# Kernel optimization log

Hardware: AMD Instinct MI355X
Metric: run time of the kernel (lower is better)

## Reference

```python
import jax, jax.numpy as jnp
import numpy as np

K = 16       # patchsize
STRIDE = 4
C1 = 1e-6
C2 = 1e-6


def _unfold(x):
    # Mirrors nn.Unfold(kernel_size=16, stride=4) followed by
    # .view(a,b,k,k,-1).transpose(2,4): output (a,b,pt_num,k,k) where the
    # trailing (k,k) matrix is the TRANSPOSED patch (kw,kh), exactly as in torch.
    a, b, H, W = x.shape
    nh = (H - K) // STRIDE + 1
    nw = (W - K) // STRIDE + 1
    r = (jnp.arange(nh) * STRIDE)[:, None] + jnp.arange(K)[None, :]  # (nh,K)
    c = (jnp.arange(nw) * STRIDE)[:, None] + jnp.arange(K)[None, :]  # (nw,K)
    p = x[:, :, r[:, None, :, None], c[None, :, None, :]]  # (a,b,nh,nw,K,K) = (kh,kw)
    p = p.reshape(a, b, nh * nw, K, K)
    return jnp.swapaxes(p, -1, -2)  # transposed patch, matching transpose(2,4)


def _layer(ref_f, dist_f):
    # ref_f, dist_f: (a,b,H,W) feature maps of one VGG layer
    pr = _unfold(ref_f)   # (a,b,pt,K,K)
    pd = _unfold(dist_f)
    u_r, s_r, _ = jnp.linalg.svd(pr, full_matrices=False)  # u:(a,b,pt,K,K) s:(a,b,pt,K)
    u_d, s_d, _ = jnp.linalg.svd(pd, full_matrices=False)
    diff_s = (s_r - s_d) ** 2                               # (a,b,pt,K)
    # abs of elementwise U product summed over singular-vector index (sign-invariant)
    u_rd = jnp.abs(u_r * u_d).sum(-1)                       # (a,b,pt,K)
    wt = jnp.std(u_rd, axis=-1, ddof=1) / (jnp.mean(u_rd, axis=-1) + 1e-9)  # (a,b,pt)
    ds = (diff_s.sum(-1) * wt).mean(-1).mean(-1)            # (a,)
    # global luminance-similarity weighting
    xm = dist_f.mean(axis=(2, 3))                           # (a,b)
    ym = ref_f.mean(axis=(2, 3))
    s1 = (2.0 * xm * ym + C1) / (xm ** 2 + ym ** 2 + C2)
    glb = jnp.exp(-2.0 * s1.mean(axis=1))                   # (a,)
    return ds * glb


def setup_inputs() -> dict:
    key = jax.random.key(0)
    k1, k2, k3, k4 = jax.random.split(key, 4)
    return {
        "ref_feat3": jax.random.normal(k1, (4, 256, 64, 64), jnp.float32),
        "dist_feat3": jax.random.normal(k2, (4, 256, 64, 64), jnp.float32),
        "ref_feat4": jax.random.normal(k3, (4, 512, 32, 32), jnp.float32),
        "dist_feat4": jax.random.normal(k4, (4, 512, 32, 32), jnp.float32),
    }


def reference(ref_feat3, dist_feat3, ref_feat4, dist_feat4):
    # DMM accumulates the weighted singular-value distance over the two feature levels
    return _layer(ref_feat3, dist_feat3) + _layer(ref_feat4, dist_feat4)
```

## Files before the change

kernel.cpp:

```cpp
#include <hip/hip_runtime.h>
#include <math.h>

#define NSWEEPS 4

typedef _Float16 f16x2 __attribute__((ext_vector_type(2)));
typedef float    f32x2 __attribute__((ext_vector_type(2)));

__device__ __forceinline__ int h2i(f16x2 v) { int r; __builtin_memcpy(&r, &v, 4); return r; }
__device__ __forceinline__ f16x2 i2h(int v) { f16x2 r; __builtin_memcpy(&r, &v, 4); return r; }
__device__ __forceinline__ f16x2 dup_h(float x) { _Float16 h = (_Float16)x; return f16x2{h, h}; }

__device__ __forceinline__ f32x2 rcp2(f32x2 v) {
  return f32x2{__builtin_amdgcn_rcpf(v.x), __builtin_amdgcn_rcpf(v.y)};
}
__device__ __forceinline__ f32x2 sqrt2(f32x2 v) {
  return f32x2{__builtin_amdgcn_sqrtf(v.x), __builtin_amdgcn_sqrtf(v.y)};
}
__device__ __forceinline__ f32x2 cpsgn2(f32x2 m, f32x2 s) {
  return f32x2{copysignf(m.x, s.x), copysignf(m.y, s.y)};
}

template<int R>
__device__ __forceinline__ int xexch_i(int iv) {
  if constexpr (R == 1)       return __builtin_amdgcn_update_dpp(iv, iv, 0x0B1, 0xF, 0xF, true);
  else if constexpr (R == 2)  return __builtin_amdgcn_update_dpp(iv, iv, 0x04E, 0xF, 0xF, true);
  else if constexpr (R == 3)  return __builtin_amdgcn_update_dpp(iv, iv, 0x01B, 0xF, 0xF, true);
  else if constexpr (R == 7)  return __builtin_amdgcn_update_dpp(iv, iv, 0x141, 0xF, 0xF, true);
  else if constexpr (R == 8)  return __builtin_amdgcn_update_dpp(iv, iv, 0x128, 0xF, 0xF, true);
  else if constexpr (R == 15) return __builtin_amdgcn_update_dpp(iv, iv, 0x140, 0xF, 0xF, true);
  else                        return __builtin_amdgcn_ds_swizzle(iv, (R << 10) | 0x1F);
}
template<int R>
__device__ __forceinline__ float xexch(float v) {
  return __int_as_float(xexch_i<R>(__float_as_int(v)));
}

template<int R>
__device__ __forceinline__ void jround2p(f16x2 (&wa)[8], f16x2 (&wb)[8],
                                         f32x2 &nn, f32x2 &d, f32x2 &id) {
  const f32x2 on = {xexch<R>(nn.x), xexch<R>(nn.y)};
  const f32x2 od = {xexch<R>(d.x),  xexch<R>(d.y)};
  f16x2 oa[8], ob[8];
#pragma unroll
  for (int i = 0; i < 8; ++i) oa[i] = i2h(xexch_i<R>(h2i(wa[i])));
#pragma unroll
  for (int i = 0; i < 8; ++i) ob[i] = i2h(xexch_i<R>(h2i(wb[i])));

  float pa0 = 0.f, pa1 = 0.f, pa2 = 0.f, pa3 = 0.f;
  float pb0 = 0.f, pb1 = 0.f, pb2 = 0.f, pb3 = 0.f;
  pa0 = __builtin_amdgcn_fdot2(wa[0], oa[0], pa0, false);
  pa1 = __builtin_amdgcn_fdot2(wa[1], oa[1], pa1, false);
  pa2 = __builtin_amdgcn_fdot2(wa[2], oa[2], pa2, false);
  pa3 = __builtin_amdgcn_fdot2(wa[3], oa[3], pa3, false);
  pb0 = __builtin_amdgcn_fdot2(wb[0], ob[0], pb0, false);
  pb1 = __builtin_amdgcn_fdot2(wb[1], ob[1], pb1, false);
  pb2 = __builtin_amdgcn_fdot2(wb[2], ob[2], pb2, false);
  pb3 = __builtin_amdgcn_fdot2(wb[3], ob[3], pb3, false);
  pa0 = __builtin_amdgcn_fdot2(wa[4], oa[4], pa0, false);
  pa1 = __builtin_amdgcn_fdot2(wa[5], oa[5], pa1, false);
  pa2 = __builtin_amdgcn_fdot2(wa[6], oa[6], pa2, false);
  pa3 = __builtin_amdgcn_fdot2(wa[7], oa[7], pa3, false);
  pb0 = __builtin_amdgcn_fdot2(wb[4], ob[4], pb0, false);
  pb1 = __builtin_amdgcn_fdot2(wb[5], ob[5], pb1, false);
  pb2 = __builtin_amdgcn_fdot2(wb[6], ob[6], pb2, false);
  pb3 = __builtin_amdgcn_fdot2(wb[7], ob[7], pb3, false);
  const f32x2 dot = {(pa0 + pa1) + (pa2 + pa3), (pb0 + pb1) + (pb2 + pb3)};

  const f32x2 dod = d * od;
  const f32x2 apq = dot * dod;
  const f32x2 dl  = on - nn;
  const f32x2 p2  = apq + apq;
  const f32x2 rt  = sqrt2(dl * dl + p2 * p2 + 1e-37f);
  const f32x2 den = dl + cpsgn2(rt, dl);
  const f32x2 t   = p2 * rcp2(den);
  const f32x2 sec = sqrt2(t * t + 1.0f);
  const f32x2 c   = rcp2(sec);
  const f32x2 rc  = -t * (id * od);

  const f16x2 ra = dup_h(rc.x);
  const f16x2 rb = dup_h(rc.y);
#pragma unroll
  for (int i = 0; i < 8; ++i) wa[i] = __builtin_elementwise_fma(ra, oa[i], wa[i]);
#pragma unroll
  for (int i = 0; i < 8; ++i) wb[i] = __builtin_elementwise_fma(rb, ob[i], wb[i]);
  d  *= c;
  id *= sec;
  nn  = nn - t * apq;
}

__device__ __forceinline__ void jrounds(f16x2 (&a)[8], f16x2 (&b)[8],
                                        f32x2 &nn, f32x2 &d, f32x2 &id) {
  jround2p<1>(a, b, nn, d, id);
  jround2p<2>(a, b, nn, d, id);
  jround2p<3>(a, b, nn, d, id);
  jround2p<4>(a, b, nn, d, id);
  jround2p<5>(a, b, nn, d, id);
  jround2p<6>(a, b, nn, d, id);
  jround2p<7>(a, b, nn, d, id);
  jround2p<8>(a, b, nn, d, id);
  jround2p<9>(a, b, nn, d, id);
  jround2p<10>(a, b, nn, d, id);
  jround2p<11>(a, b, nn, d, id);
  jround2p<12>(a, b, nn, d, id);
  jround2p<13>(a, b, nn, d, id);
  jround2p<14>(a, b, nn, d, id);
  jround2p<15>(a, b, nn, d, id);
}

__device__ __forceinline__ void load16(const float* __restrict__ src, float (&a)[16]) {
  const float4* p = (const float4*)src;
  float4 v0 = p[0], v1 = p[1], v2 = p[2], v3 = p[3];
  a[0] = v0.x; a[1] = v0.y; a[2]  = v0.z; a[3]  = v0.w;
  a[4] = v1.x; a[5] = v1.y; a[6]  = v1.z; a[7]  = v1.w;
  a[8] = v2.x; a[9] = v2.y; a[10] = v2.z; a[11] = v2.w;
  a[12] = v3.x; a[13] = v3.y; a[14] = v3.z; a[15] = v3.w;
}

template<int R>
__device__ __forceinline__ void rankstep(float s2, int lane, int &rank) {
  const float vk = xexch<R>(s2);
  rank += (vk > s2 || (vk == s2 && (lane ^ R) < lane)) ? 1 : 0;
}
__device__ __forceinline__ int rank16(float s2, int lane) {
  int rank = 0;
  rankstep<1>(s2, lane, rank);  rankstep<2>(s2, lane, rank);
  rankstep<3>(s2, lane, rank);  rankstep<4>(s2, lane, rank);
  rankstep<5>(s2, lane, rank);  rankstep<6>(s2, lane, rank);
  rankstep<7>(s2, lane, rank);  rankstep<8>(s2, lane, rank);
  rankstep<9>(s2, lane, rank);  rankstep<10>(s2, lane, rank);
  rankstep<11>(s2, lane, rank); rankstep<12>(s2, lane, rank);
  rankstep<13>(s2, lane, rank); rankstep<14>(s2, lane, rank);
  rankstep<15>(s2, lane, rank);
  return rank;
}

__device__ __forceinline__ float sort16p(f16x2 (&u)[8], float s2,
                                         const int lane, const int wl) {
  const int rank = rank16(s2, lane);
  const int dst = (((wl & 48) | rank) << 2);
#pragma unroll
  for (int i = 0; i < 8; ++i)
    u[i] = i2h(__builtin_amdgcn_ds_permute(dst, h2i(u[i])));
  return __int_as_float(__builtin_amdgcn_ds_permute(dst, __float_as_int(s2)));
}

template<int CH, int H, int W, int NH, int NW>
__global__ __launch_bounds__(256)
void svd_layer_kernel(const float* __restrict__ ref, const float* __restrict__ dist,
                      float* __restrict__ dsSum) {
  constexpr int P = NH * NW;
  const int tid  = threadIdx.x;
  const int lane = tid & 15;
  const int wl   = tid & 63;
  const int pid  = blockIdx.x * 16 + (tid >> 4);
  const int ai   = pid / (CH * P);
  const int rem  = pid - ai * (CH * P);
  const int ch   = rem / P;
  const int pp   = rem - ch * P;
  const int ih   = pp / NW;
  const int iw   = pp - ih * NW;
  const size_t off = (size_t)(ai * CH + ch) * (H * W) + (size_t)(ih * 4 + lane) * W + iw * 4;

  float tr[16], td[16];
  load16(ref + off, tr);
  load16(dist + off, td);

  float nnr = 0.f, nnd = 0.f;
#pragma unroll
  for (int i = 0; i < 16; ++i) { nnr = fmaf(tr[i], tr[i], nnr); nnd = fmaf(td[i], td[i], nnd); }

  f16x2 wr[8], wd[8];
#pragma unroll
  for (int i = 0; i < 8; ++i) {
    wr[i] = f16x2{(_Float16)tr[2 * i], (_Float16)tr[2 * i + 1]};
    wd[i] = f16x2{(_Float16)td[2 * i], (_Float16)td[2 * i + 1]};
  }

  f32x2 nn = {nnr, nnd};
  f32x2 d  = {1.f, 1.f};
  f32x2 id = {1.f, 1.f};
#pragma unroll
  for (int sw = 0; sw < NSWEEPS; ++sw) {
    jrounds(wr, wd, nn, d, id);
    if (sw < NSWEEPS - 1) {
      const f16x2 sa = dup_h(d.x), sb = dup_h(d.y);
#pragma unroll
      for (int i = 0; i < 8; ++i) { wr[i] *= sa; wd[i] *= sb; }
      d = f32x2{1.f, 1.f}; id = f32x2{1.f, 1.f};
    }
  }

  float r0 = 0.f, r1 = 0.f, q0 = 0.f, q1 = 0.f;
#pragma unroll
  for (int i = 0; i < 8; i += 2) {
    r0 = __builtin_amdgcn_fdot2(wr[i],     wr[i],     r0, false);
    r1 = __builtin_amdgcn_fdot2(wr[i + 1], wr[i + 1], r1, false);
    q0 = __builtin_amdgcn_fdot2(wd[i],     wd[i],     q0, false);
    q1 = __builtin_amdgcn_fdot2(wd[i + 1], wd[i + 1], q1, false);
  }
  const float sw2r = r0 + r1, sw2d = q0 + q1;
  float s2r = sw2r * (d.x * d.x);
  float s2d = sw2d * (d.y * d.y);
  const f16x2 ur_s = dup_h(__builtin_amdgcn_rsqf(sw2r + 1e-30f));
  const f16x2 ud_s = dup_h(__builtin_amdgcn_rsqf(sw2d + 1e-30f));
#pragma unroll
  for (int i = 0; i < 8; ++i) { wr[i] *= ur_s; wd[i] *= ud_s; }

  s2r = sort16p(wr, s2r, lane, wl);
  s2d = sort16p(wd, s2d, lane, wl);

  const float sigr = __builtin_amdgcn_sqrtf(s2r);
  const float sigd = __builtin_amdgcn_sqrtf(s2d);
  const float ddv = sigr - sigd;
  float diffs = ddv * ddv;
  diffs += xexch<1>(diffs);
  diffs += xexch<2>(diffs);
  diffs += xexch<4>(diffs);
  diffs += xexch<8>(diffs);

  f16x2 prd[8];
#pragma unroll
  for (int i = 0; i < 8; ++i) prd[i] = i2h(h2i(wr[i] * wd[i]) & 0x7FFF7FFF);
#pragma unroll
  for (int i = 0; i < 8; ++i) prd[i] += i2h(xexch_i<1>(h2i(prd[i])));
#pragma unroll
  for (int i = 0; i < 8; ++i) prd[i] += i2h(xexch_i<2>(h2i(prd[i])));
#pragma unroll
  for (int i = 0; i < 8; ++i) prd[i] += i2h(xexch_i<4>(h2i(prd[i])));
#pragma unroll
  for (int i = 0; i < 8; ++i) prd[i] += i2h(xexch_i<8>(h2i(prd[i])));
  const f16x2 one2 = {(_Float16)1.f, (_Float16)1.f};
  float sA0 = 0.f, sA1 = 0.f, sQ0 = 0.f, sQ1 = 0.f;
#pragma unroll
  for (int i = 0; i < 8; i += 2) {
    sA0 = __builtin_amdgcn_fdot2(prd[i],     one2,       sA0, false);
    sA1 = __builtin_amdgcn_fdot2(prd[i + 1], one2,       sA1, false);
    sQ0 = __builtin_amdgcn_fdot2(prd[i],     prd[i],     sQ0, false);
    sQ1 = __builtin_amdgcn_fdot2(prd[i + 1], prd[i + 1], sQ1, false);
  }
  const float sum = sA0 + sA1, sumsq = sQ0 + sQ1;
  const float mean = sum * 0.0625f;
  float var = (sumsq - 16.0f * mean * mean) * (1.0f / 15.0f);
  var = fmaxf(var, 0.0f);
  const float wt  = __builtin_amdgcn_sqrtf(var) * __builtin_amdgcn_rcpf(mean + 1e-9f);
  const float val = diffs * wt;

  __shared__ float blk;
  if (tid == 0) blk = 0.0f;
  __syncthreads();
  if (lane == 0) atomicAdd(&blk, val);
  __syncthreads();
  if (tid == 0) atomicAdd(&dsSum[ai], blk);
}

template<int CH, int HW>
__global__ __launch_bounds__(256)
void glb_kernel(const float* __restrict__ ref, const float* __restrict__ dist,
                float* __restrict__ s1Sum) {
  const int bid = blockIdx.x;
  const int ai  = bid / CH;
  const float4* pr = (const float4*)(ref + (size_t)bid * HW);
  const float4* pd = (const float4*)(dist + (size_t)bid * HW);
  float sr = 0.0f, sd = 0.0f;
  for (int i = threadIdx.x; i < HW / 4; i += 256) {
    const float4 r = pr[i], d = pd[i];
    sr += (r.x + r.y) + (r.z + r.w);
    sd += (d.x + d.y) + (d.z + d.w);
  }
#pragma unroll
  for (int st = 32; st >= 1; st >>= 1) { sr += __shfl_xor(sr, st, 64); sd += __shfl_xor(sd, st, 64); }
  __shared__ float bufR[4], bufD[4];
  const int w = threadIdx.x >> 6;
  if ((threadIdx.x & 63) == 0) { bufR[w] = sr; bufD[w] = sd; }
  __syncthreads();
  if (threadIdx.x == 0) {
    const float ym = (bufR[0] + bufR[1] + bufR[2] + bufR[3]) * (1.0f / HW);
    const float xm = (bufD[0] + bufD[1] + bufD[2] + bufD[3]) * (1.0f / HW);
    const float s1 = (2.0f * xm * ym + 1e-6f) / (xm * xm + ym * ym + 1e-6f);
    atomicAdd(&s1Sum[ai], s1);
  }
}

__global__ void final_kernel(const float* __restrict__ ws, float* __restrict__ out) {
  const int ai = threadIdx.x;
  if (ai < 4) {
    const float ds3 = ws[ai]      * (1.0f / (256.0f * 169.0f));
    const float ds4 = ws[4 + ai]  * (1.0f / (512.0f * 25.0f));
    const float g3  = expf(-2.0f * ws[8 + ai]  * (1.0f / 256.0f));
    const float g4  = expf(-2.0f * ws[12 + ai] * (1.0f / 512.0f));
    out[ai] = ds3 * g3 + ds4 * g4;
  }
}

extern "C" void kernel_launch(void* const* d_in, const int* in_sizes, int n_in,
                              void* d_out, int out_size, void* d_ws, size_t ws_size,
                              hipStream_t stream) {
  const float* ref3  = (const float*)d_in[0];
  const float* dist3 = (const float*)d_in[1];
  const float* ref4  = (const float*)d_in[2];
  const float* dist4 = (const float*)d_in[3];
  float* ws  = (float*)d_ws;
  float* out = (float*)d_out;

  hipMemsetAsync(ws, 0, 16 * sizeof(float), stream);

  svd_layer_kernel<256, 64, 64, 13, 13><<<173056 / 16, 256, 0, stream>>>(ref3, dist3, ws + 0);
  svd_layer_kernel<512, 32, 32, 5, 5><<<51200 / 16, 256, 0, stream>>>(ref4, dist4, ws + 4);

  glb_kernel<256, 4096><<<4 * 256, 256, 0, stream>>>(ref3, dist3, ws + 8);
  glb_kernel<512, 1024><<<4 * 512, 256, 0, stream>>>(ref4, dist4, ws + 12);

  final_kernel<<<1, 64, 0, stream>>>(ws, out);
}
```

Before: 678.1 us.

## Cross-assign ref/dist matrices by lane parity to halve odd-distance Jacobi dot products

Measured after the change: 643.0 us. -5.2%, faster.

```diff
diff --git a/kernel.cpp b/kernel.cpp
--- a/kernel.cpp
+++ b/kernel.cpp
@@ -36,35 +36,61 @@
 }
 
 template<int R>
-__device__ __forceinline__ void jround2p(f16x2 (&wa)[8], f16x2 (&wb)[8],
+__device__ __forceinline__ void jround2p(f16x2 (&X)[8], f16x2 (&Y)[8],
                                          f32x2 &nn, f32x2 &d, f32x2 &id) {
-  const f32x2 on = {xexch<R>(nn.x), xexch<R>(nn.y)};
-  const f32x2 od = {xexch<R>(d.x),  xexch<R>(d.y)};
-  f16x2 oa[8], ob[8];
-#pragma unroll
-  for (int i = 0; i < 8; ++i) oa[i] = i2h(xexch_i<R>(h2i(wa[i])));
-#pragma unroll
-  for (int i = 0; i < 8; ++i) ob[i] = i2h(xexch_i<R>(h2i(wb[i])));
-
-  float pa0 = 0.f, pa1 = 0.f, pa2 = 0.f, pa3 = 0.f;
-  float pb0 = 0.f, pb1 = 0.f, pb2 = 0.f, pb3 = 0.f;
-  pa0 = __builtin_amdgcn_fdot2(wa[0], oa[0], pa0, false);
-  pa1 = __builtin_amdgcn_fdot2(wa[1], oa[1], pa1, false);
-  pa2 = __builtin_amdgcn_fdot2(wa[2], oa[2], pa2, false);
-  pa3 = __builtin_amdgcn_fdot2(wa[3], oa[3], pa3, false);
-  pb0 = __builtin_amdgcn_fdot2(wb[0], ob[0], pb0, false);
-  pb1 = __builtin_amdgcn_fdot2(wb[1], ob[1], pb1, false);
-  pb2 = __builtin_amdgcn_fdot2(wb[2], ob[2], pb2, false);
-  pb3 = __builtin_amdgcn_fdot2(wb[3], ob[3], pb3, false);
-  pa0 = __builtin_amdgcn_fdot2(wa[4], oa[4], pa0, false);
-  pa1 = __builtin_amdgcn_fdot2(wa[5], oa[5], pa1, false);
-  pa2 = __builtin_amdgcn_fdot2(wa[6], oa[6], pa2, false);
-  pa3 = __builtin_amdgcn_fdot2(wa[7], oa[7], pa3, false);
-  pb0 = __builtin_amdgcn_fdot2(wb[4], ob[4], pb0, false);
-  pb1 = __builtin_amdgcn_fdot2(wb[5], ob[5], pb1, false);
-  pb2 = __builtin_amdgcn_fdot2(wb[6], ob[6], pb2, false);
-  pb3 = __builtin_amdgcn_fdot2(wb[7], ob[7], pb3, false);
-  const f32x2 dot = {(pa0 + pa1) + (pa2 + pa3), (pb0 + pb1) + (pb2 + pb3)};
+  constexpr bool SPLIT = (__builtin_popcount(R) & 1) != 0;
+  f32x2 on, od;
+  f16x2 oX[8], oY[8];
+  if constexpr (SPLIT) {
+    on = f32x2{xexch<R>(nn.y), xexch<R>(nn.x)};
+    od = f32x2{xexch<R>(d.y),  xexch<R>(d.x)};
+#pragma unroll
+    for (int i = 0; i < 8; ++i) oX[i] = i2h(xexch_i<R>(h2i(Y[i])));
+#pragma unroll
+    for (int i = 0; i < 8; ++i) oY[i] = i2h(xexch_i<R>(h2i(X[i])));
+  } else {
+    on = f32x2{xexch<R>(nn.x), xexch<R>(nn.y)};
+    od = f32x2{xexch<R>(d.x),  xexch<R>(d.y)};
+#pragma unroll
+    for (int i = 0; i < 8; ++i) oX[i] = i2h(xexch_i<R>(h2i(X[i])));
+#pragma unroll
+    for (int i = 0; i < 8; ++i) oY[i] = i2h(xexch_i<R>(h2i(Y[i])));
+  }
+
+  f32x2 dot;
+  if constexpr (SPLIT) {
+    float p0 = 0.f, p1 = 0.f, q0 = 0.f, q1 = 0.f;
+    p0 = __builtin_amdgcn_fdot2(X[0], oX[0], p0, false);
+    p1 = __builtin_amdgcn_fdot2(X[1], oX[1], p1, false);
+    q0 = __builtin_amdgcn_fdot2(X[2], oX[2], q0, false);
+    q1 = __builtin_amdgcn_fdot2(X[3], oX[3], q1, false);
+    p0 = __builtin_amdgcn_fdot2(X[4], oX[4], p0, false);
+    p1 = __builtin_amdgcn_fdot2(X[5], oX[5], p1, false);
+    q0 = __builtin_amdgcn_fdot2(X[6], oX[6], q0, false);
+    q1 = __builtin_amdgcn_fdot2(X[7], oX[7], q1, false);
+    const float dx = (p0 + p1) + (q0 + q1);
+    dot = f32x2{dx, xexch<R>(dx)};
+  } else {
+    float pa0 = 0.f, pa1 = 0.f, pa2 = 0.f, pa3 = 0.f;
+    float pb0 = 0.f, pb1 = 0.f, pb2 = 0.f, pb3 = 0.f;
+    pa0 = __builtin_amdgcn_fdot2(X[0], oX[0], pa0, false);
+    pa1 = __builtin_amdgcn_fdot2(X[1], oX[1], pa1, false);
+    pa2 = __builtin_amdgcn_fdot2(X[2], oX[2], pa2, false);
+    pa3 = __builtin_amdgcn_fdot2(X[3], oX[3], pa3, false);
+    pb0 = __builtin_amdgcn_fdot2(Y[0], oY[0], pb0, false);
+    pb1 = __builtin_amdgcn_fdot2(Y[1], oY[1], pb1, false);
+    pb2 = __builtin_amdgcn_fdot2(Y[2], oY[2], pb2, false);
+    pb3 = __builtin_amdgcn_fdot2(Y[3], oY[3], pb3, false);
+    pa0 = __builtin_amdgcn_fdot2(X[4], oX[4], pa0, false);
+    pa1 = __builtin_amdgcn_fdot2(X[5], oX[5], pa1, false);
+    pa2 = __builtin_amdgcn_fdot2(X[6], oX[6], pa2, false);
+    pa3 = __builtin_amdgcn_fdot2(X[7], oX[7], pa3, false);
+    pb0 = __builtin_amdgcn_fdot2(Y[4], oY[4], pb0, false);
+    pb1 = __builtin_amdgcn_fdot2(Y[5], oY[5], pb1, false);
+    pb2 = __builtin_amdgcn_fdot2(Y[6], oY[6], pb2, false);
+    pb3 = __builtin_amdgcn_fdot2(Y[7], oY[7], pb3, false);
+    dot = f32x2{(pa0 + pa1) + (pa2 + pa3), (pb0 + pb1) + (pb2 + pb3)};
+  }
 
   const f32x2 dod = d * od;
   const f32x2 apq = dot * dod;
@@ -80,31 +106,31 @@
   const f16x2 ra = dup_h(rc.x);
   const f16x2 rb = dup_h(rc.y);
 #pragma unroll
-  for (int i = 0; i < 8; ++i) wa[i] = __builtin_elementwise_fma(ra, oa[i], wa[i]);
-#pragma unroll
-  for (int i = 0; i < 8; ++i) wb[i] = __builtin_elementwise_fma(rb, ob[i], wb[i]);
+  for (int i = 0; i < 8; ++i) X[i] = __builtin_elementwise_fma(ra, oX[i], X[i]);
+#pragma unroll
+  for (int i = 0; i < 8; ++i) Y[i] = __builtin_elementwise_fma(rb, oY[i], Y[i]);
   d  *= c;
   id *= sec;
   nn  = nn - t * apq;
 }
 
-__device__ __forceinline__ void jrounds(f16x2 (&a)[8], f16x2 (&b)[8],
+__device__ __forceinline__ void jrounds(f16x2 (&X)[8], f16x2 (&Y)[8],
                                         f32x2 &nn, f32x2 &d, f32x2 &id) {
-  jround2p<1>(a, b, nn, d, id);
-  jround2p<2>(a, b, nn, d, id);
-  jround2p<3>(a, b, nn, d, id);
-  jround2p<4>(a, b, nn, d, id);
-  jround2p<5>(a, b, nn, d, id);
-  jround2p<6>(a, b, nn, d, id);
-  jround2p<7>(a, b, nn, d, id);
-  jround2p<8>(a, b, nn, d, id);
-  jround2p<9>(a, b, nn, d, id);
-  jround2p<10>(a, b, nn, d, id);
-  jround2p<11>(a, b, nn, d, id);
-  jround2p<12>(a, b, nn, d, id);
-  jround2p<13>(a, b, nn, d, id);
-  jround2p<14>(a, b, nn, d, id);
-  jround2p<15>(a, b, nn, d, id);
+  jround2p<1>(X, Y, nn, d, id);
+  jround2p<2>(X, Y, nn, d, id);
+  jround2p<3>(X, Y, nn, d, id);
+  jround2p<4>(X, Y, nn, d, id);
+  jround2p<5>(X, Y, nn, d, id);
+  jround2p<6>(X, Y, nn, d, id);
+  jround2p<7>(X, Y, nn, d, id);
+  jround2p<8>(X, Y, nn, d, id);
+  jround2p<9>(X, Y, nn, d, id);
+  jround2p<10>(X, Y, nn, d, id);
+  jround2p<11>(X, Y, nn, d, id);
+  jround2p<12>(X, Y, nn, d, id);
+  jround2p<13>(X, Y, nn, d, id);
+  jround2p<14>(X, Y, nn, d, id);
+  jround2p<15>(X, Y, nn, d, id);
 }
 
 __device__ __forceinline__ void load16(const float* __restrict__ src, float (&a)[16]) {
@@ -169,23 +195,25 @@
 #pragma unroll
   for (int i = 0; i < 16; ++i) { nnr = fmaf(tr[i], tr[i], nnr); nnd = fmaf(td[i], td[i], nnd); }
 
-  f16x2 wr[8], wd[8];
+  const bool po = (__popc(lane) & 1) != 0;
+  f16x2 X[8], Y[8];
 #pragma unroll
   for (int i = 0; i < 8; ++i) {
-    wr[i] = f16x2{(_Float16)tr[2 * i], (_Float16)tr[2 * i + 1]};
-    wd[i] = f16x2{(_Float16)td[2 * i], (_Float16)td[2 * i + 1]};
-  }
-
-  f32x2 nn = {nnr, nnd};
+    const f16x2 hr = f16x2{(_Float16)tr[2 * i], (_Float16)tr[2 * i + 1]};
+    const f16x2 hd = f16x2{(_Float16)td[2 * i], (_Float16)td[2 * i + 1]};
+    X[i] = po ? hd : hr;
+    Y[i] = po ? hr : hd;
+  }
+  f32x2 nn = po ? f32x2{nnd, nnr} : f32x2{nnr, nnd};
   f32x2 d  = {1.f, 1.f};
   f32x2 id = {1.f, 1.f};
 #pragma unroll
   for (int sw = 0; sw < NSWEEPS; ++sw) {
-    jrounds(wr, wd, nn, d, id);
+    jrounds(X, Y, nn, d, id);
     if (sw < NSWEEPS - 1) {
       const f16x2 sa = dup_h(d.x), sb = dup_h(d.y);
 #pragma unroll
-      for (int i = 0; i < 8; ++i) { wr[i] *= sa; wd[i] *= sb; }
+      for (int i = 0; i < 8; ++i) { X[i] *= sa; Y[i] *= sb; }
       d = f32x2{1.f, 1.f}; id = f32x2{1.f, 1.f};
     }
   }
@@ -193,18 +221,25 @@
   float r0 = 0.f, r1 = 0.f, q0 = 0.f, q1 = 0.f;
 #pragma unroll
   for (int i = 0; i < 8; i += 2) {
-    r0 = __builtin_amdgcn_fdot2(wr[i],     wr[i],     r0, false);
-    r1 = __builtin_amdgcn_fdot2(wr[i + 1], wr[i + 1], r1, false);
-    q0 = __builtin_amdgcn_fdot2(wd[i],     wd[i],     q0, false);
-    q1 = __builtin_amdgcn_fdot2(wd[i + 1], wd[i + 1], q1, false);
-  }
-  const float sw2r = r0 + r1, sw2d = q0 + q1;
-  float s2r = sw2r * (d.x * d.x);
-  float s2d = sw2d * (d.y * d.y);
-  const f16x2 ur_s = dup_h(__builtin_amdgcn_rsqf(sw2r + 1e-30f));
-  const f16x2 ud_s = dup_h(__builtin_amdgcn_rsqf(sw2d + 1e-30f));
-#pragma unroll
-  for (int i = 0; i < 8; ++i) { wr[i] *= ur_s; wd[i] *= ud_s; }
+    r0 = __builtin_amdgcn_fdot2(X[i],     X[i],     r0, false);
+    r1 = __builtin_amdgcn_fdot2(X[i + 1], X[i + 1], r1, false);
+    q0 = __builtin_amdgcn_fdot2(Y[i],     Y[i],     q0, false);
+    q1 = __builtin_amdgcn_fdot2(Y[i + 1], Y[i + 1], q1, false);
+  }
+  const float sw2X = r0 + r1, sw2Y = q0 + q1;
+  const float s2X = sw2X * (d.x * d.x);
+  const float s2Y = sw2Y * (d.y * d.y);
+  const f16x2 uX_s = dup_h(__builtin_amdgcn_rsqf(sw2X + 1e-30f));
+  const f16x2 uY_s = dup_h(__builtin_amdgcn_rsqf(sw2Y + 1e-30f));
+  f16x2 wr[8], wd[8];
+#pragma unroll
+  for (int i = 0; i < 8; ++i) {
+    const f16x2 ux = X[i] * uX_s, uy = Y[i] * uY_s;
+    wr[i] = po ? uy : ux;
+    wd[i] = po ? ux : uy;
+  }
+  float s2r = po ? s2Y : s2X;
+  float s2d = po ? s2X : s2Y;
 
   s2r = sort16p(wr, s2r, lane, wl);
   s2d = sort16p(wd, s2d, lane, wl);
@@ -253,19 +288,22 @@
   if (tid == 0) atomicAdd(&dsSum[ai], blk);
 }
 
-template<int CH, int HW>
 __global__ __launch_bounds__(256)
-void glb_kernel(const float* __restrict__ ref, const float* __restrict__ dist,
-                float* __restrict__ s1Sum) {
-  const int bid = blockIdx.x;
-  const int ai  = bid / CH;
+void glb2_kernel(const float* __restrict__ ref3, const float* __restrict__ dist3,
+                 const float* __restrict__ ref4, const float* __restrict__ dist4,
+                 float* __restrict__ ws) {
+  const int b = blockIdx.x;
+  const float* ref; const float* dist; float* s1; int CH, HW, bid;
+  if (b < 1024) { ref = ref3; dist = dist3; s1 = ws + 8;  CH = 256; HW = 4096; bid = b; }
+  else          { ref = ref4; dist = dist4; s1 = ws + 12; CH = 512; HW = 1024; bid = b - 1024; }
+  const int ai = bid / CH;
   const float4* pr = (const float4*)(ref + (size_t)bid * HW);
   const float4* pd = (const float4*)(dist + (size_t)bid * HW);
   float sr = 0.0f, sd = 0.0f;
   for (int i = threadIdx.x; i < HW / 4; i += 256) {
-    const float4 r = pr[i], d = pd[i];
+    const float4 r = pr[i], dv = pd[i];
     sr += (r.x + r.y) + (r.z + r.w);
-    sd += (d.x + d.y) + (d.z + d.w);
+    sd += (dv.x + dv.y) + (dv.z + dv.w);
   }
 #pragma unroll
   for (int st = 32; st >= 1; st >>= 1) { sr += __shfl_xor(sr, st, 64); sd += __shfl_xor(sd, st, 64); }
@@ -274,10 +312,11 @@
   if ((threadIdx.x & 63) == 0) { bufR[w] = sr; bufD[w] = sd; }
   __syncthreads();
   if (threadIdx.x == 0) {
-    const float ym = (bufR[0] + bufR[1] + bufR[2] + bufR[3]) * (1.0f / HW);
-    const float xm = (bufD[0] + bufD[1] + bufD[2] + bufD[3]) * (1.0f / HW);
-    const float s1 = (2.0f * xm * ym + 1e-6f) / (xm * xm + ym * ym + 1e-6f);
-    atomicAdd(&s1Sum[ai], s1);
+    const float inv = 1.0f / (float)HW;
+    const float ym = (bufR[0] + bufR[1] + bufR[2] + bufR[3]) * inv;
+    const float xm = (bufD[0] + bufD[1] + bufD[2] + bufD[3]) * inv;
+    const float s1v = (2.0f * xm * ym + 1e-6f) / (xm * xm + ym * ym + 1e-6f);
+    atomicAdd(&s1[ai], s1v);
   }
 }
 
@@ -307,8 +346,6 @@
   svd_layer_kernel<256, 64, 64, 13, 13><<<173056 / 16, 256, 0, stream>>>(ref3, dist3, ws + 0);
   svd_layer_kernel<512, 32, 32, 5, 5><<<51200 / 16, 256, 0, stream>>>(ref4, dist4, ws + 4);
 
-  glb_kernel<256, 4096><<<4 * 256, 256, 0, stream>>>(ref3, dist3, ws + 8);
-  glb_kernel<512, 1024><<<4 * 512, 256, 0, stream>>>(ref4, dist4, ws + 12);
-
+  glb2_kernel<<<1024 + 2048, 256, 0, stream>>>(ref3, dist3, ref4, dist4, ws);
   final_kernel<<<1, 64, 0, stream>>>(ws, out);
 }
```
